# Kernel tuning notes

Measured on AMD Instinct MI355X. Metric: run time of the kernel, lower is better.

The kernel has to match this reference:

```python
import jax, jax.numpy as jnp
import numpy as np
from functools import partial

GRID = 5  # 224/32 - 2
N_ANCHORS = 3
N_BOX = GRID * GRID * N_ANCHORS  # 75


def _make_anchors():
    # faithful replication of _create_anchors (grid-index cx,cy with pixel-scale w,h)
    scales = [56, 112, 224]
    a = np.zeros((GRID, GRID, N_ANCHORS, 8), np.float32)
    for x in range(GRID):
        for y in range(GRID):
            for k in range(N_ANCHORS):
                w = h = scales[k]
                a[x, y, k] = [x - w // 2, y - h // 2, x + w // 2, y + h // 2, x, y, w, h]
    return jnp.asarray(a)

ANCHORS = _make_anchors()  # [5,5,3,8]: x0,y0,x1,y1,cx,cy,w,h


def conv2d(x, w, b, pad):
    y = jax.lax.conv_general_dilated(x, w, (1, 1), [(pad, pad), (pad, pad)],
                                     dimension_numbers=('NCHW', 'OIHW', 'NCHW'))
    return y + b[None, :, None, None]


def maxpool2(x):
    return jax.lax.reduce_window(x, -jnp.inf, jax.lax.max,
                                 (1, 1, 2, 2), (1, 1, 2, 2), 'VALID')


def deparam_bboxes(rp_reg):
    # rp_reg: [B,5,5,3,4]; anchors broadcast over batch
    aw = ANCHORS[..., 6]; ah = ANCHORS[..., 7]
    ax = ANCHORS[..., 4]; ay = ANCHORS[..., 5]
    cx = rp_reg[..., 0] * aw + ax
    cy = rp_reg[..., 1] * ah + ay
    w = jnp.exp(rp_reg[..., 2]) * aw
    h = jnp.exp(rp_reg[..., 3]) * ah
    return jnp.stack([cx - w / 2, cy - h / 2, cx + w / 2, cy + h / 2], axis=-1)


def _iou_as_written(bi, bj):
    # replicates bb_intersection_over_union EXACTLY, including the missing
    # parentheses bug: inter/areaA + areaB - inter
    xA = jnp.maximum(bi[0], bj[..., 0]); yA = jnp.maximum(bi[1], bj[..., 1])
    xB = jnp.minimum(bi[2], bj[..., 2]); yB = jnp.minimum(bi[3], bj[..., 3])
    inter = jnp.maximum(0.0, xB - xA + 1) * jnp.maximum(0.0, yB - yA + 1)
    areaA = (bi[2] - bi[0] + 1) * (bi[3] - bi[1] + 1)
    areaB = (bj[..., 2] - bj[..., 0] + 1) * (bj[..., 3] - bj[..., 1] + 1)
    return inter / areaA + areaB - inter


def nms_single(boxes, scores, thresh=0.7):
    # boxes [75,4], scores [75]; greedy suppression in score order (vectorized
    # replacement of the O(n^2) Python-loop NMS in _compute_bboxes)
    order = jnp.argsort(-scores)
    b = boxes[order]
    idx = jnp.arange(N_BOX)

    def body(i, keep):
        iou = _iou_as_written(b[i], b)          # [75]
        sup = (idx > i) & (iou > thresh) & keep[i]
        return keep & ~sup

    keep_sorted = jax.lax.fori_loop(0, N_BOX, body, jnp.ones(N_BOX, bool))
    return jnp.zeros(N_BOX, bool).at[order].set(keep_sorted)


def setup_inputs() -> dict:
    key = jax.random.key(0)
    ks = jax.random.split(key, 16)
    B = 32
    inp = {"x": jax.random.normal(ks[0], (B, 3, 224, 224), jnp.float32)}
    chans = [3, 64, 128, 256, 512, 512]
    for i in range(5):
        cin, cout = chans[i], chans[i + 1]
        std = float(np.sqrt(2.0 / (cout * 9)))  # kaiming fan_out, relu
        inp[f"fw{i}"] = jax.random.normal(ks[1 + i], (cout, cin, 3, 3), jnp.float32) * std
        inp[f"fb{i}"] = jnp.zeros((cout,), jnp.float32)
    # RPN heads: normal(0, 0.01), zero bias (per _initialize_rp_weights)
    inp["rpw_w"] = jax.random.normal(ks[6], (512, 512, 3, 3), jnp.float32) * 0.01
    inp["rpw_b"] = jnp.zeros((512,), jnp.float32)
    inp["cls_w"] = jax.random.normal(ks[7], (N_ANCHORS, 512, 1, 1), jnp.float32) * 0.01
    inp["cls_b"] = jnp.zeros((N_ANCHORS,), jnp.float32)
    inp["reg_w"] = jax.random.normal(ks[8], (4 * N_ANCHORS, 512, 1, 1), jnp.float32) * 0.01
    inp["reg_b"] = jnp.zeros((4 * N_ANCHORS,), jnp.float32)
    # classifier2: Linear(512*7*7, 20), normal(0, 0.01)
    inp["fc_w"] = jax.random.normal(ks[9], (20, 512 * 7 * 7), jnp.float32) * 0.01
    inp["fc_b"] = jnp.zeros((20,), jnp.float32)
    return inp


def reference(x, fw0, fb0, fw1, fb1, fw2, fb2, fw3, fb3, fw4, fb4,
              rpw_w, rpw_b, cls_w, cls_b, reg_w, reg_b, fc_w, fc_b):
    B = x.shape[0]
    feat = x
    for w, b in ((fw0, fb0), (fw1, fb1), (fw2, fb2), (fw3, fb3), (fw4, fb4)):
        feat = maxpool2(jax.nn.relu(conv2d(feat, w, b, pad=1)))
    # feat: [B,512,7,7]
    rp512 = jax.nn.relu(conv2d(feat, rpw_w, rpw_b, pad=0))          # [B,512,5,5]
    rp_cls = jax.nn.sigmoid(conv2d(rp512, cls_w, cls_b, pad=0))     # [B,3,5,5]
    rp_reg = conv2d(rp512, reg_w, reg_b, pad=0)                     # [B,12,5,5]
    # faithful to torch .view (row-major reshape, NOT permute)
    rp_cls = rp_cls.reshape(B, GRID, GRID, N_ANCHORS)
    rp_reg = rp_reg.reshape(B, GRID, GRID, N_ANCHORS, 4)
    bboxes = deparam_bboxes(rp_reg)                                 # [B,5,5,3,4]
    keep = jax.vmap(nms_single)(bboxes.reshape(B, N_BOX, 4),
                                rp_cls.reshape(B, N_BOX))           # [B,75] bool
    logits = feat.reshape(B, -1) @ fc_w.T + fc_b                    # [B,20]
    return logits, rp_cls, rp_reg, bboxes, keep
```

## Files before the change

### kernel.cpp

```cpp
#include <hip/hip_runtime.h>
#include <math.h>


#define OFF_LOGITS 0
#define OFF_CLS    640
#define OFF_REG    3040
#define OFF_BOXES  12640
#define OFF_KEEP   22240

constexpr int BATCH = 32;

typedef _Float16 h8 __attribute__((ext_vector_type(8)));
typedef _Float16 h4 __attribute__((ext_vector_type(4)));
typedef float    f4 __attribute__((ext_vector_type(4)));

#define MFMA16(a, b, c) __builtin_amdgcn_mfma_f32_16x16x32_f16(a, b, c, 0, 0, 0)

#if defined(__has_builtin)
#  if __has_builtin(__builtin_amdgcn_global_load_lds)
#    define HAS_GLL 1
#  endif
#endif

__device__ __forceinline__ void stage16(const _Float16* g, _Float16* lbase, int lane) {
#ifdef HAS_GLL
  __builtin_amdgcn_global_load_lds((const __attribute__((address_space(1))) void*)g,
                                   (__attribute__((address_space(3))) void*)lbase,
                                   16, 0, 0);
#else
  *reinterpret_cast<h8*>(lbase + lane * 8) = *reinterpret_cast<const h8*>(g);
#endif
}

constexpr size_t A_OFF = 0;
constexpr size_t B_OFF = 106463232;
constexpr size_t W_OFF = 161579008;
constexpr size_t P_OFF = A_OFF + 8388608;

constexpr int I0_E = 26615808;
constexpr int I1_E = 13778944;
constexpr int I2_E = 7372800;
constexpr int I3_E = 4194304;
constexpr int I4_E = 802816;

__global__ __launch_bounds__(256)
void wcvt(const float* __restrict__ src, _Float16* __restrict__ dHi,
          _Float16* __restrict__ dLo, int COUT, int CIN) {
  const int total = COUT * CIN * 9;
  for (int idx = blockIdx.x * 256 + threadIdx.x; idx < total; idx += gridDim.x * 256) {
    const int co = idx / (CIN * 9);
    const int r = idx % (CIN * 9);
    const int ci = r / 9, tap = r % 9;
    const float v = src[idx];
    const _Float16 h = (_Float16)v;
    const int o = ((tap * (CIN >> 5) + (ci >> 5)) * COUT + co) * 32 + (ci & 31);
    dHi[o] = h;
    dLo[o] = (_Float16)(v - (float)h);
  }
}

__global__ __launch_bounds__(256)
void zero_ring(_Float16* __restrict__ hi, _Float16* __restrict__ lo, int P, int C) {
  const int c8n = C / 8, cells = 4 * P - 4;
  const int tot = 32 * cells * c8n;
  for (int idx = blockIdx.x * 256 + threadIdx.x; idx < tot; idx += gridDim.x * 256) {
    const int c8 = idx % c8n;
    const int cell = (idx / c8n) % cells;
    const int n = idx / (c8n * cells);
    int y, xx;
    if (cell < 2 * P) { y = (cell < P) ? 0 : (P - 1); xx = cell % P; }
    else { const int q = cell - 2 * P; y = 1 + (q >> 1); xx = (q & 1) ? (P - 1) : 0; }
    const long o = ((long)(n * P + y) * P + xx) * C + c8 * 8;
    h8 z = {};
    *reinterpret_cast<h8*>(hi + o) = z;
    *reinterpret_cast<h8*>(lo + o) = z;
  }
}

constexpr int L0_SW   = 0;
constexpr int L0_SB   = 6912;
constexpr int L0_SIN  = 7168;
constexpr int L0_HI   = 7168;
constexpr int L0_LO   = 7168 + 36864;
constexpr int L0_LDS  = 7168 + 73728;

__global__ __launch_bounds__(256)
void conv_l0(const float* __restrict__ x, const float* __restrict__ w0,
             const float* __restrict__ b0, _Float16* __restrict__ outHi,
             _Float16* __restrict__ outLo) {
  const int bid = blockIdx.x;
  const int tx0 = (bid % 7) * 16, ty0 = ((bid / 7) % 7) * 16, n = bid / 49;
  __align__(16) __shared__ char lds[L0_LDS];
  float* sW = (float*)(lds + L0_SW);
  float* sB = (float*)(lds + L0_SB);
  float* sIn = (float*)(lds + L0_SIN);
  const int tid = threadIdx.x;
  for (int idx = tid; idx < 3 * 34 * 34; idx += 256) {
    const int ci = idx / 1156, rem = idx % 1156, r = rem / 34, cc = rem % 34;
    const int y = 2 * ty0 - 1 + r, xx = 2 * tx0 - 1 + cc;
    float v = 0.f;
    if ((unsigned)y < 224u && (unsigned)xx < 224u)
      v = x[((n * 3 + ci) * 224 + y) * 224 + xx];
    sIn[idx] = v;
  }
  for (int idx = tid; idx < 1728; idx += 256) sW[idx] = w0[idx];
  if (tid < 64) sB[tid] = b0[tid];
  __syncthreads();

  const int tpy = tid / 16, tpx = tid % 16;
  float win[3][4][4];
  #pragma unroll
  for (int ci = 0; ci < 3; ++ci)
    #pragma unroll
    for (int dr = 0; dr < 4; ++dr)
      #pragma unroll
      for (int dc = 0; dc < 4; ++dc)
        win[ci][dr][dc] = sIn[ci * 1156 + (2 * tpy + dr) * 34 + (2 * tpx + dc)];
  __syncthreads();

  for (int co4 = 0; co4 < 16; ++co4) {
    h4 hh, ll;
    #pragma unroll
    for (int j = 0; j < 4; ++j) {
      const int co = co4 * 4 + j;
      float a00 = 0.f, a01 = 0.f, a10 = 0.f, a11 = 0.f;
      #pragma unroll
      for (int ci = 0; ci < 3; ++ci)
        #pragma unroll
        for (int ky = 0; ky < 3; ++ky)
          #pragma unroll
          for (int kx = 0; kx < 3; ++kx) {
            const float wv = sW[co * 27 + ci * 9 + ky * 3 + kx];
            a00 = fmaf(win[ci][ky][kx], wv, a00);
            a01 = fmaf(win[ci][ky][kx + 1], wv, a01);
            a10 = fmaf(win[ci][ky + 1][kx], wv, a10);
            a11 = fmaf(win[ci][ky + 1][kx + 1], wv, a11);
          }
      const float p = fmaxf(fmaxf(fmaxf(a00, a01), fmaxf(a10, a11)) + sB[co], 0.f);
      const _Float16 h = (_Float16)p;
      hh[j] = h;
      ll[j] = (_Float16)(p - (float)h);
    }
    *reinterpret_cast<h4*>(lds + L0_HI + tid * 144 + co4 * 8) = hh;
    *reinterpret_cast<h4*>(lds + L0_LO + tid * 144 + co4 * 8) = ll;
  }
  __syncthreads();

  const int tr_half = tid >> 7;
  const int pixrow = (tid & 127) >> 3;
  const int ch8 = (tid & 7) * 8;
  #pragma unroll
  for (int i = 0; i < 8; ++i) {
    const int tr = 2 * i + tr_half;
    const int pix = tr * 16 + pixrow;
    const long ga = ((long)(n * 114 + ty0 + tr + 1) * 114 + tx0 + pixrow + 1) * 64 + ch8;
    *reinterpret_cast<h8*>(outHi + ga) =
        *reinterpret_cast<const h8*>(lds + L0_HI + pix * 144 + ch8 * 2);
    *reinterpret_cast<h8*>(outLo + ga) =
        *reinterpret_cast<const h8*>(lds + L0_LO + pix * 144 + ch8 * 2);
  }
}

template<int CIN, int COUT, int H, int XH, int NCOW, int STG, int SARR>
__global__ __launch_bounds__(256, 2)
void convrow(const _Float16* __restrict__ inHi, const _Float16* __restrict__ inLo,
             const _Float16* __restrict__ wHi, const _Float16* __restrict__ wLo,
             const float* __restrict__ bias, _Float16* __restrict__ outHi,
             _Float16* __restrict__ outLo) {
  constexpr int W = H, Hp = H / 2, Wp = W / 2, PW = W + 2, POW = Wp + 2;
  constexpr int KCH = CIN / 32;
  constexpr int NPH = 3 * KCH;
  constexpr int NSPW = 4 / NCOW;
  constexpr int NFULL = STG / 64;
  constexpr int TAIL = STG % 64;
  static_assert(NSPW * 64 + 3 < STG + 1, "staged rows cover shifted reads");
  __align__(16) __shared__ _Float16 sB[2][2][SARR * 32];

  const int tid = threadIdx.x;
  const int lane = tid & 63, wv = tid >> 6;
  const int c = lane & 15, kq = lane >> 4;
  const int cow = blockIdx.y * (NCOW * 64) + (wv % NCOW) * 64;
  const int spl = (wv / NCOW) * 64;
  const int xh = blockIdx.x % XH;
  const int pyn = blockIdx.x / XH;
  const int py = pyn % Hp, n = pyn / Hp;
  const int x0 = xh * 64;

  int gstage[NFULL + 1];
  #pragma unroll
  for (int i = 0; i < NFULL + 1; ++i) {
    const int sl = i * 64 + tid / 4;
    const int ry = sl & 1;
    int xx = x0 + (sl >> 1);
    if (xx > PW - 1) xx = PW - 1;
    gstage[i] = ((n * (H + 2) + 2 * py + ry) * PW + xx) * CIN +
                (((tid & 3) ^ ((sl >> 1) & 3)) * 8);
  }
  int dsoff[3][4];
  #pragma unroll
  for (int kx = 0; kx < 3; ++kx)
    #pragma unroll
    for (int nt = 0; nt < 4; ++nt) {
      const int r = spl + nt * 16 + c + 2 * kx;
      dsoff[kx][nt] = r * 32 + ((kq ^ ((r >> 1) & 3)) * 8);
    }

  #pragma unroll
  for (int i = 0; i < NFULL; ++i) {
    stage16(inHi + gstage[i], &sB[0][0][i * 2048 + wv * 512], lane);
    stage16(inLo + gstage[i], &sB[0][1][i * 2048 + wv * 512], lane);
  }
  if (TAIL && tid < TAIL * 4) {
    stage16(inHi + gstage[NFULL], &sB[0][0][NFULL * 2048], lane);
    stage16(inLo + gstage[NFULL], &sB[0][1][NFULL * 2048], lane);
  }
  __syncthreads();

  f4 acc[4][4] = {};
  int cur = 0;
  for (int ph = 0; ph < NPH; ++ph) {
    const int ky = ph / KCH, kc = ph % KCH;
    if (ph + 1 < NPH) {
      const int tb2 = ((ph + 1) / KCH) * PW * CIN + ((ph + 1) % KCH) * 32;
      #pragma unroll
      for (int i = 0; i < NFULL; ++i) {
        stage16(inHi + gstage[i] + tb2, &sB[cur ^ 1][0][i * 2048 + wv * 512], lane);
        stage16(inLo + gstage[i] + tb2, &sB[cur ^ 1][1][i * 2048 + wv * 512], lane);
      }
      if (TAIL && tid < TAIL * 4) {
        stage16(inHi + gstage[NFULL] + tb2, &sB[cur ^ 1][0][NFULL * 2048], lane);
        stage16(inLo + gstage[NFULL] + tb2, &sB[cur ^ 1][1][NFULL * 2048], lane);
      }
    }
    #pragma unroll
    for (int kx = 0; kx < 3; ++kx) {
      h8 aH[4], aL[4];
      const long abase = ((long)((ky * 3 + kx) * KCH + kc) * COUT + cow) * 32;
      #pragma unroll
      for (int mt = 0; mt < 4; ++mt) {
        const long ao = abase + (mt * 16 + c) * 32 + kq * 8;
        aH[mt] = *reinterpret_cast<const h8*>(wHi + ao);
        aL[mt] = *reinterpret_cast<const h8*>(wLo + ao);
      }
      h8 bH[4], bL[4];
      #pragma unroll
      for (int nt = 0; nt < 4; ++nt) {
        bH[nt] = *reinterpret_cast<const h8*>(&sB[cur][0][dsoff[kx][nt]]);
        bL[nt] = *reinterpret_cast<const h8*>(&sB[cur][1][dsoff[kx][nt]]);
      }
      __builtin_amdgcn_s_setprio(1);
      #pragma unroll
      for (int mt = 0; mt < 4; ++mt)
        #pragma unroll
        for (int nt = 0; nt < 4; ++nt)
          acc[mt][nt] = MFMA16(aH[mt], bH[nt], acc[mt][nt]);
      #pragma unroll
      for (int mt = 0; mt < 4; ++mt)
        #pragma unroll
        for (int nt = 0; nt < 4; ++nt)
          acc[mt][nt] = MFMA16(aH[mt], bL[nt], acc[mt][nt]);
      #pragma unroll
      for (int mt = 0; mt < 4; ++mt)
        #pragma unroll
        for (int nt = 0; nt < 4; ++nt)
          acc[mt][nt] = MFMA16(aL[mt], bH[nt], acc[mt][nt]);
      __builtin_amdgcn_s_setprio(0);
    }
    __syncthreads();
    cur ^= 1;
  }

  const int r4 = lane >> 4;
  #pragma unroll
  for (int mt = 0; mt < 4; ++mt) {
    const int co0 = cow + mt * 16 + r4 * 4;
    const f4 bi = *reinterpret_cast<const f4*>(bias + co0);
    #pragma unroll
    for (int nt = 0; nt < 4; ++nt) {
      f4 v = acc[mt][nt];
      #pragma unroll
      for (int r = 0; r < 4; ++r) {
        const float m1 = fmaxf(v[r], __shfl_xor(v[r], 1, 64));
        v[r] = fmaxf(m1, __shfl_xor(m1, 2, 64));
      }
      if ((lane & 3) == 0) {
        const int rr = spl + nt * 16 + c;
        const int pxg = xh * 32 + (rr >> 2);
        if (pxg < Wp) {
          h4 hh, ll;
          #pragma unroll
          for (int r = 0; r < 4; ++r) {
            const float p = fmaxf(v[r] + bi[r], 0.f);
            const _Float16 h = (_Float16)p;
            hh[r] = h;
            ll[r] = (_Float16)(p - (float)h);
          }
          const long oa = ((long)((n * (Hp + 2) + py + 1) * POW + pxg + 1)) * COUT + co0;
          *reinterpret_cast<h4*>(outHi + oa) = hh;
          *reinterpret_cast<h4*>(outLo + oa) = ll;
        }
      }
    }
  }
}

template<int CIN, int COUT, int H, int BCO, int BSP, int TG, int KPH, int MODE>
__global__ __launch_bounds__(256, 2)
void convpool(const _Float16* __restrict__ inHi, const _Float16* __restrict__ inLo,
              const _Float16* __restrict__ wHi, const _Float16* __restrict__ wLo,
              const float* __restrict__ bias, _Float16* __restrict__ outHi,
              _Float16* __restrict__ outLo, float* __restrict__ outF) {
  constexpr int W = H, Hp = H / 2, Wp = W / 2, PW = W + 2, POW = Wp + 2;
  constexpr int NCOW = BCO / 64, NSPW = BSP / 64;
  static_assert(NCOW * NSPW == 4, "4 waves");
  constexpr int KCH = CIN / 32;
  constexpr int NCH = TG * KCH;
  constexpr int NPH = NCH / KPH;
  static_assert(NCH % KPH == 0, "even phases");
  static_assert(KPH * 2 * (BSP / 64) == 4, "prologue vmcnt literal = 4");
  constexpr int NISS = BSP / 64;
  constexpr int SPTOT = 32 * H * W;
  constexpr int TSZ = BSP * 32;
  __align__(16) __shared__ _Float16 sB[3 * 2 * KPH * TSZ];
  #define TIDX(buf, hl, j) ((((buf) * 2 + (hl)) * KPH + (j)) * TSZ)

  const int tid = threadIdx.x;
  const int lane = tid & 63, wv = tid >> 6;
  const int c = lane & 15, kq = lane >> 4;
  const int cow = blockIdx.y * BCO + (wv % NCOW) * 64;
  const int spl = (wv / NCOW) * 64;
  const int sblk = blockIdx.x * BSP;
  const int tap0 = (TG == 9) ? 0 : blockIdx.z * TG;

  int gstage[NISS];
  #pragma unroll
  for (int i = 0; i < NISS; ++i) {
    const int sl = i * 64 + tid / 4;
    const int sg = sblk + sl;
    const int ry = sg & 1, tt = sg >> 1;
    const int x = tt % W, u = tt / W;
    const int py = u % Hp, n = u / Hp;
    gstage[i] = ((n * (H + 2) + 2 * py + ry) * PW + x) * CIN +
                (((tid & 3) ^ ((sl >> 1) & 3)) * 8);
  }
  int dsoff[4];
  #pragma unroll
  for (int nt = 0; nt < 4; ++nt) {
    const int row = spl + nt * 16 + c;
    dsoff[nt] = row * 32 + ((kq ^ ((row >> 1) & 3)) * 8);
  }

  #pragma unroll
  for (int pp = 0; pp < 2; ++pp) {
    #pragma unroll
    for (int j = 0; j < KPH; ++j) {
      const int ch = pp * KPH + j;
      const int tap = tap0 + ch / KCH, kc = ch % KCH;
      const int tb = ((tap / 3) * PW + (tap % 3)) * CIN + kc * 32;
      #pragma unroll
      for (int i = 0; i < NISS; ++i) {
        stage16(inHi + gstage[i] + tb, &sB[TIDX(pp, 0, j) + i * 2048 + wv * 512], lane);
        stage16(inLo + gstage[i] + tb, &sB[TIDX(pp, 1, j) + i * 2048 + wv * 512], lane);
      }
    }
  }
  __builtin_amdgcn_sched_barrier(0);
  asm volatile("s_waitcnt vmcnt(4)" ::: "memory");
  __builtin_amdgcn_sched_barrier(0);
  __builtin_amdgcn_s_barrier();
  __builtin_amdgcn_sched_barrier(0);

  f4 acc[4][4] = {};
  for (int ph = 0; ph < NPH; ++ph) {
    const int bp = ph % 3;
    h8 aH[KPH][4], aL[KPH][4];
    #pragma unroll
    for (int j = 0; j < KPH; ++j) {
      const int ch = ph * KPH + j;
      const int tap = tap0 + ch / KCH;
      const int kc = ch % KCH;
      const long abase = ((long)(tap * KCH + kc) * COUT + cow) * 32;
      #pragma unroll
      for (int mt = 0; mt < 4; ++mt) {
        const long ao = abase + (mt * 16 + c) * 32 + kq * 8;
        aH[j][mt] = *reinterpret_cast<const h8*>(wHi + ao);
        aL[j][mt] = *reinterpret_cast<const h8*>(wLo + ao);
      }
    }
    __builtin_amdgcn_sched_barrier(0);
    if (ph + 2 < NPH) {
      const int bs = (ph + 2) % 3;
      #pragma unroll
      for (int j2 = 0; j2 < KPH; ++j2) {
        const int ch2 = (ph + 2) * KPH + j2;
        const int tap2 = tap0 + ch2 / KCH;
        const int tb2 = ((tap2 / 3) * PW + (tap2 % 3)) * CIN + (ch2 % KCH) * 32;
        #pragma unroll
        for (int i = 0; i < NISS; ++i) {
          stage16(inHi + gstage[i] + tb2,
                  &sB[TIDX(bs, 0, j2) + i * 2048 + wv * 512], lane);
          stage16(inLo + gstage[i] + tb2,
                  &sB[TIDX(bs, 1, j2) + i * 2048 + wv * 512], lane);
        }
      }
    }
    __builtin_amdgcn_sched_barrier(0);
    #pragma unroll
    for (int j = 0; j < KPH; ++j) {
      h8 bH[4], bL[4];
      #pragma unroll
      for (int nt = 0; nt < 4; ++nt) {
        bH[nt] = *reinterpret_cast<const h8*>(&sB[TIDX(bp, 0, j) + dsoff[nt]]);
        bL[nt] = *reinterpret_cast<const h8*>(&sB[TIDX(bp, 1, j) + dsoff[nt]]);
      }
      __builtin_amdgcn_s_setprio(1);
      #pragma unroll
      for (int mt = 0; mt < 4; ++mt)
        #pragma unroll
        for (int nt = 0; nt < 4; ++nt)
          acc[mt][nt] = MFMA16(aH[j][mt], bH[nt], acc[mt][nt]);
      #pragma unroll
      for (int mt = 0; mt < 4; ++mt)
        #pragma unroll
        for (int nt = 0; nt < 4; ++nt)
          acc[mt][nt] = MFMA16(aH[j][mt], bL[nt], acc[mt][nt]);
      #pragma unroll
      for (int mt = 0; mt < 4; ++mt)
        #pragma unroll
        for (int nt = 0; nt < 4; ++nt)
          acc[mt][nt] = MFMA16(aL[j][mt], bH[nt], acc[mt][nt]);
      __builtin_amdgcn_s_setprio(0);
    }
    __builtin_amdgcn_sched_barrier(0);
    __builtin_amdgcn_s_barrier();
    __builtin_amdgcn_sched_barrier(0);
  }
  #undef TIDX

  const int r4 = lane >> 4;
  if (MODE == 1) {
    #pragma unroll
    for (int mt = 0; mt < 4; ++mt) {
      const int co0 = cow + mt * 16 + r4 * 4;
      #pragma unroll
      for (int nt = 0; nt < 4; ++nt) {
        const int s = sblk + spl + nt * 16 + c;
        *reinterpret_cast<f4*>(outF + ((long)blockIdx.z * SPTOT + s) * COUT + co0) =
            acc[mt][nt];
      }
    }
  } else {
    #pragma unroll
    for (int mt = 0; mt < 4; ++mt) {
      const int co0 = cow + mt * 16 + r4 * 4;
      const f4 bi = *reinterpret_cast<const f4*>(bias + co0);
      #pragma unroll
      for (int nt = 0; nt < 4; ++nt) {
        f4 v = acc[mt][nt];
        #pragma unroll
        for (int r = 0; r < 4; ++r) {
          const float m1 = fmaxf(v[r], __shfl_xor(v[r], 1, 64));
          v[r] = fmaxf(m1, __shfl_xor(m1, 2, 64));
        }
        if ((lane & 3) == 0) {
          const int s = sblk + spl + nt * 16 + c;
          const int ps = s >> 2;
          const int n = ps / (Hp * Wp), rem = ps % (Hp * Wp);
          const int py = rem / Wp, px = rem % Wp;
          h4 hh, ll;
          #pragma unroll
          for (int r = 0; r < 4; ++r) {
            const float p = fmaxf(v[r] + bi[r], 0.f);
            const _Float16 h = (_Float16)p;
            hh[r] = h;
            ll[r] = (_Float16)(p - (float)h);
          }
          const long oa = ((long)((n * (Hp + 2) + py + 1) * POW + px + 1)) * COUT + co0;
          *reinterpret_cast<h4*>(outHi + oa) = hh;
          *reinterpret_cast<h4*>(outLo + oa) = ll;
        }
      }
    }
  }
}

__global__ __launch_bounds__(256)
void l4_finish(const float* __restrict__ part, const float* __restrict__ bias,
               _Float16* __restrict__ I4h, _Float16* __restrict__ I4l,
               float* __restrict__ feat) {
  const int t = blockIdx.x * 256 + threadIdx.x;
  if (t >= 1568 * 128) return;
  const int co0 = (t % 128) * 4, p = t / 128;
  f4 m;
  #pragma unroll
  for (int q = 0; q < 4; ++q) {
    const long s = 4L * p + q;
    f4 v = *reinterpret_cast<const f4*>(part + s * 512 + co0);
    v += *reinterpret_cast<const f4*>(part + (6272 + s) * 512 + co0);
    v += *reinterpret_cast<const f4*>(part + (12544 + s) * 512 + co0);
    if (q == 0) m = v;
    else {
      #pragma unroll
      for (int r = 0; r < 4; ++r) m[r] = fmaxf(m[r], v[r]);
    }
  }
  const f4 bi = *reinterpret_cast<const f4*>(bias + co0);
  h4 hh, ll;
  const int n = p / 49, pix = p % 49;
  #pragma unroll
  for (int r = 0; r < 4; ++r) {
    const float pv = fmaxf(m[r] + bi[r], 0.f);
    const _Float16 h = (_Float16)pv;
    hh[r] = h;
    ll[r] = (_Float16)(pv - (float)h);
    feat[((long)(n * 512 + co0 + r)) * 49 + pix] = pv;
  }
  *reinterpret_cast<h4*>(I4h + (long)p * 512 + co0) = hh;
  *reinterpret_cast<h4*>(I4l + (long)p * 512 + co0) = ll;
}

__global__ __launch_bounds__(256)
void rpn_partial(const _Float16* __restrict__ inHi, const _Float16* __restrict__ inLo,
                 const _Float16* __restrict__ wHi, const _Float16* __restrict__ wLo,
                 float* __restrict__ part) {
  const int lane = threadIdx.x & 63, wv = threadIdx.x >> 6;
  const int cow = blockIdx.y * 128 + wv * 32;
  const int sblk = blockIdx.x * 64;
  const int tap = blockIdx.z, ky = tap / 3, kx = tap % 3;
  const int c = lane & 15, kq = lane >> 4;

  int baseB[4];
  #pragma unroll
  for (int nt = 0; nt < 4; ++nt) {
    int s = sblk + nt * 16 + c;
    if (s > 799) s = 799;
    const int n = s / 25, pix = s % 25, py = pix / 5, px = pix % 5;
    baseB[nt] = ((n * 7 + py + ky) * 7 + px + kx) * 512;
  }

  f4 acc[2][4] = {};
  for (int kch = 0; kch < 16; ++kch) {
    h8 aH[2], aL[2], bH[4], bL[4];
    const long abase = ((long)(tap * 16 + kch) * 512 + cow) * 32;
    #pragma unroll
    for (int mt = 0; mt < 2; ++mt) {
      const long ao = abase + (mt * 16 + c) * 32 + kq * 8;
      aH[mt] = *reinterpret_cast<const h8*>(wHi + ao);
      aL[mt] = *reinterpret_cast<const h8*>(wLo + ao);
    }
    #pragma unroll
    for (int nt = 0; nt < 4; ++nt) {
      const int bo = baseB[nt] + kch * 32 + kq * 8;
      bH[nt] = *reinterpret_cast<const h8*>(inHi + bo);
      bL[nt] = *reinterpret_cast<const h8*>(inLo + bo);
    }
    #pragma unroll
    for (int mt = 0; mt < 2; ++mt)
      #pragma unroll
      for (int nt = 0; nt < 4; ++nt)
        acc[mt][nt] = MFMA16(aH[mt], bH[nt], acc[mt][nt]);
    #pragma unroll
    for (int mt = 0; mt < 2; ++mt)
      #pragma unroll
      for (int nt = 0; nt < 4; ++nt)
        acc[mt][nt] = MFMA16(aH[mt], bL[nt], acc[mt][nt]);
    #pragma unroll
    for (int mt = 0; mt < 2; ++mt)
      #pragma unroll
      for (int nt = 0; nt < 4; ++nt)
        acc[mt][nt] = MFMA16(aL[mt], bH[nt], acc[mt][nt]);
  }

  const int r4 = lane >> 4;
  #pragma unroll
  for (int mt = 0; mt < 2; ++mt) {
    const int co0 = cow + mt * 16 + r4 * 4;
    #pragma unroll
    for (int nt = 0; nt < 4; ++nt) {
      const int s = sblk + nt * 16 + c;
      if (s < 800)
        *reinterpret_cast<f4*>(part + ((long)tap * 800 + s) * 512 + co0) = acc[mt][nt];
    }
  }
}

__global__ __launch_bounds__(256)
void rpn_finish(const float* __restrict__ part, const float* __restrict__ bias,
                float* __restrict__ rp512) {
  const int t = blockIdx.x * 256 + threadIdx.x;
  if (t >= 800 * 128) return;
  const int co0 = (t % 128) * 4, s = t / 128;
  f4 acc = *reinterpret_cast<const f4*>(bias + co0);
  #pragma unroll
  for (int g = 0; g < 9; ++g)
    acc += *reinterpret_cast<const f4*>(part + ((long)g * 800 + s) * 512 + co0);
  f4 o;
  #pragma unroll
  for (int r = 0; r < 4; ++r) o[r] = fmaxf(acc[r], 0.f);
  *reinterpret_cast<f4*>(rp512 + (long)s * 512 + co0) = o;
}

__global__ __launch_bounds__(256)
void heads_kernel(const float* __restrict__ rp512,
                  const float* __restrict__ cls_w, const float* __restrict__ cls_b,
                  const float* __restrict__ reg_w, const float* __restrict__ reg_b,
                  float* __restrict__ out) {
  const int idx = blockIdx.x * 256 + threadIdx.x;
  if (idx >= 32 * 25 * 15) return;
  const int o = idx % 15, pix = (idx / 15) % 25, n = idx / 375;
  const float* __restrict__ ip = rp512 + ((long)(n * 25 + pix)) * 512;
  const float* __restrict__ wvp = (o < 3) ? (cls_w + o * 512) : (reg_w + (o - 3) * 512);
  float acc = 0.f;
  for (int k = 0; k < 512; k += 4) {
    const f4 a = *reinterpret_cast<const f4*>(ip + k);
    const f4 b = *reinterpret_cast<const f4*>(wvp + k);
    acc = fmaf(a[0], b[0], acc); acc = fmaf(a[1], b[1], acc);
    acc = fmaf(a[2], b[2], acc); acc = fmaf(a[3], b[3], acc);
  }
  if (o < 3) {
    acc += cls_b[o];
    out[OFF_CLS + n * 75 + o * 25 + pix] = 1.f / (1.f + expf(-acc));
  } else {
    acc += reg_b[o - 3];
    out[OFF_REG + n * 300 + (o - 3) * 25 + pix] = acc;
  }
}

__global__ __launch_bounds__(256)
void fc_kernel(const float* __restrict__ feat, const float* __restrict__ fw,
               const float* __restrict__ fb, float* __restrict__ out) {
  const int n = blockIdx.x, j = blockIdx.y;
  const float* __restrict__ ip = feat + (long)n * 25088;
  const float* __restrict__ wj = fw + (long)j * 25088;
  float acc = 0.f;
  for (int k = threadIdx.x * 4; k < 25088; k += 1024) {
    const f4 a = *reinterpret_cast<const f4*>(ip + k);
    const f4 b = *reinterpret_cast<const f4*>(wj + k);
    acc = fmaf(a[0], b[0], acc); acc = fmaf(a[1], b[1], acc);
    acc = fmaf(a[2], b[2], acc); acc = fmaf(a[3], b[3], acc);
  }
  #pragma unroll
  for (int m = 32; m >= 1; m >>= 1) acc += __shfl_xor(acc, m, 64);
  __shared__ float red[4];
  const int wv = threadIdx.x >> 6;
  if ((threadIdx.x & 63) == 0) red[wv] = acc;
  __syncthreads();
  if (threadIdx.x == 0)
    out[OFF_LOGITS + n * 20 + j] = red[0] + red[1] + red[2] + red[3] + fb[j];
}

__global__ __launch_bounds__(128)
void bbox_nms_kernel(float* __restrict__ out) {
  const int n = blockIdx.x;
  const int t = threadIdx.x;
  __shared__ float bx0[75], by0[75], bx1[75], by1[75], area[75], sc[75];
  __shared__ int rank_s[75], order_s[75], keep_s[75];

  if (t < 75) {
    const int g1 = t / 15, g2 = (t / 3) % 5, a = t % 3;
    const float aw = (a == 0) ? 56.f : (a == 1 ? 112.f : 224.f);
    const float r0 = out[OFF_REG + n * 300 + 4 * t + 0];
    const float r1 = out[OFF_REG + n * 300 + 4 * t + 1];
    const float r2 = out[OFF_REG + n * 300 + 4 * t + 2];
    const float r3 = out[OFF_REG + n * 300 + 4 * t + 3];
    const float cx = r0 * aw + (float)g1;
    const float cy = r1 * aw + (float)g2;
    const float w_ = expf(r2) * aw;
    const float h_ = expf(r3) * aw;
    const float x0 = cx - 0.5f * w_, y0 = cy - 0.5f * h_;
    const float x1 = cx + 0.5f * w_, y1 = cy + 0.5f * h_;
    bx0[t] = x0; by0[t] = y0; bx1[t] = x1; by1[t] = y1;
    area[t] = (x1 - x0 + 1.f) * (y1 - y0 + 1.f);
    out[OFF_BOXES + n * 300 + 4 * t + 0] = x0;
    out[OFF_BOXES + n * 300 + 4 * t + 1] = y0;
    out[OFF_BOXES + n * 300 + 4 * t + 2] = x1;
    out[OFF_BOXES + n * 300 + 4 * t + 3] = y1;
    sc[t] = out[OFF_CLS + n * 75 + t];
    keep_s[t] = 1;
  }
  __syncthreads();
  if (t < 75) {
    const float si = sc[t];
    int rk = 0;
    for (int j = 0; j < 75; ++j) {
      const float sj = sc[j];
      rk += (sj > si) || (sj == si && j < t);
    }
    rank_s[t] = rk;
    order_s[rk] = t;
  }
  __syncthreads();
  for (int i = 0; i < 74; ++i) {
    if (keep_s[i]) {
      const int bi = order_s[i];
      if (t > i && t < 75) {
        const int bj = order_s[t];
        const float xA = fmaxf(bx0[bi], bx0[bj]);
        const float yA = fmaxf(by0[bi], by0[bj]);
        const float xB = fminf(bx1[bi], bx1[bj]);
        const float yB = fminf(by1[bi], by1[bj]);
        const float inter = fmaxf(0.f, xB - xA + 1.f) * fmaxf(0.f, yB - yA + 1.f);
        const float iou = inter / area[bi] + area[bj] - inter;
        if (iou > 0.7f) keep_s[t] = 0;
      }
    }
    __syncthreads();
  }
  if (t < 75) out[OFF_KEEP + n * 75 + t] = keep_s[rank_s[t]] ? 1.f : 0.f;
}

extern "C" void kernel_launch(void* const* d_in, const int* in_sizes, int n_in,
                              void* d_out, int out_size, void* d_ws, size_t ws_size,
                              hipStream_t stream) {
  (void)in_sizes; (void)n_in; (void)out_size; (void)ws_size;
  const float* x     = (const float*)d_in[0];
  const float* fw0   = (const float*)d_in[1];
  const float* fb0   = (const float*)d_in[2];
  const float* fw1   = (const float*)d_in[3];
  const float* fb1   = (const float*)d_in[4];
  const float* fw2   = (const float*)d_in[5];
  const float* fb2   = (const float*)d_in[6];
  const float* fw3   = (const float*)d_in[7];
  const float* fb3   = (const float*)d_in[8];
  const float* fw4   = (const float*)d_in[9];
  const float* fb4   = (const float*)d_in[10];
  const float* rpw_w = (const float*)d_in[11];
  const float* rpw_b = (const float*)d_in[12];
  const float* cls_w = (const float*)d_in[13];
  const float* cls_b = (const float*)d_in[14];
  const float* reg_w = (const float*)d_in[15];
  const float* reg_b = (const float*)d_in[16];
  const float* fc_w  = (const float*)d_in[17];
  const float* fc_b  = (const float*)d_in[18];
  float* out = (float*)d_out;
  char* ws = (char*)d_ws;

  _Float16* I0h = (_Float16*)(ws + A_OFF);
  _Float16* I0l = I0h + I0_E;
  _Float16* I1h = (_Float16*)(ws + B_OFF);
  _Float16* I1l = I1h + I1_E;
  _Float16* I2h = (_Float16*)(ws + A_OFF);
  _Float16* I2l = I2h + I2_E;
  _Float16* I3h = (_Float16*)(ws + B_OFF);
  _Float16* I3l = I3h + I3_E;
  _Float16* I4h = (_Float16*)(ws + A_OFF);
  _Float16* I4l = I4h + I4_E;
  float* feat  = (float*)(ws + A_OFF + (size_t)I4_E * 4);
  float* rp512 = (float*)(ws + A_OFF + (size_t)I4_E * 4 + 3211264);
  float* part  = (float*)(ws + P_OFF);

  _Float16* w1h = (_Float16*)(ws + W_OFF);                _Float16* w1l = w1h + 73728;
  _Float16* w2h = (_Float16*)(ws + W_OFF + 294912);       _Float16* w2l = w2h + 294912;
  _Float16* w3h = (_Float16*)(ws + W_OFF + 1474560);      _Float16* w3l = w3h + 1179648;
  _Float16* w4h = (_Float16*)(ws + W_OFF + 6193152);      _Float16* w4l = w4h + 2359296;
  _Float16* wrh = (_Float16*)(ws + W_OFF + 15630336);     _Float16* wrl = wrh + 2359296;

  wcvt<<<(73728 + 255) / 256, 256, 0, stream>>>(fw1, w1h, w1l, 128, 64);
  wcvt<<<(294912 + 255) / 256, 256, 0, stream>>>(fw2, w2h, w2l, 256, 128);
  wcvt<<<(1179648 + 255) / 256, 256, 0, stream>>>(fw3, w3h, w3l, 512, 256);
  wcvt<<<(2359296 + 255) / 256, 256, 0, stream>>>(fw4, w4h, w4l, 512, 512);
  wcvt<<<(2359296 + 255) / 256, 256, 0, stream>>>(rpw_w, wrh, wrl, 512, 512);

  zero_ring<<<512, 256, 0, stream>>>(I0h, I0l, 114, 64);
  zero_ring<<<512, 256, 0, stream>>>(I1h, I1l, 58, 128);

  conv_l0<<<32 * 49, 256, 0, stream>>>(x, fw0, fb0, I0h, I0l);

  convrow<64, 128, 112, 2, 2, 132, 136><<<dim3(32 * 56 * 2, 1), 256, 0, stream>>>(
      I0h, I0l, w1h, w1l, fb1, I1h, I1l);
  zero_ring<<<512, 256, 0, stream>>>(I2h, I2l, 30, 256);
  convrow<128, 256, 56, 1, 2, 132, 136><<<dim3(32 * 28, 2), 256, 0, stream>>>(
      I1h, I1l, w2h, w2l, fb2, I2h, I2l);
  zero_ring<<<512, 256, 0, stream>>>(I3h, I3l, 16, 512);
  convrow<256, 512, 28, 1, 4, 68, 72><<<dim3(32 * 14, 2), 256, 0, stream>>>(
      I2h, I2l, w3h, w3l, fb3, I3h, I3l);
  convpool<512, 512, 14, 256, 64, 3, 2, 1><<<dim3(98, 2, 3), 256, 0, stream>>>(
      I3h, I3l, w4h, w4l, nullptr, nullptr, nullptr, part);
  l4_finish<<<(1568 * 128 + 255) / 256, 256, 0, stream>>>(part, fb4, I4h, I4l, feat);

  rpn_partial<<<dim3(13, 4, 9), 256, 0, stream>>>(I4h, I4l, wrh, wrl, part);
  rpn_finish<<<(800 * 128 + 255) / 256, 256, 0, stream>>>(part, rpw_b, rp512);

  heads_kernel<<<(12000 + 255) / 256, 256, 0, stream>>>(rp512, cls_w, cls_b, reg_w, reg_b, out);
  fc_kernel<<<dim3(32, 20), 256, 0, stream>>>(feat, fc_w, fc_b, out);
  bbox_nms_kernel<<<BATCH, 128, 0, stream>>>(out);
}
```

Baseline: 865.9 us.

## Widen convrow tiles so each block covers full COUT and row width

The convrow kernel drops the x-half and output-channel grid splits, so each block now computes a full pooled output row across all output channels. Each wave holds 8 M-tiles (128 channels), which raises reuse of each LDS-staged input fragment and cuts repeated staging of the same input rows across blocks. The MFMA passes are split into a bH phase and a bL phase with sched barriers to limit live registers. The cost is a larger accumulator footprint, more register pressure and far fewer blocks, which may underfill the GPU on the deeper layers. Layer 1 also needs a bigger LDS staging area.

```diff
diff --git a/kernel.cpp b/kernel.cpp
--- a/kernel.cpp
+++ b/kernel.cpp
@@ -161,7 +161,7 @@
   }
 }
 
-template<int CIN, int COUT, int H, int XH, int NCOW, int STG, int SARR>
+template<int CIN, int COUT, int H, int NCOW, int STG, int SARR>
 __global__ __launch_bounds__(256, 2)
 void convrow(const _Float16* __restrict__ inHi, const _Float16* __restrict__ inLo,
              const _Float16* __restrict__ wHi, const _Float16* __restrict__ wLo,
@@ -169,29 +169,27 @@
              _Float16* __restrict__ outLo) {
   constexpr int W = H, Hp = H / 2, Wp = W / 2, PW = W + 2, POW = Wp + 2;
   constexpr int KCH = CIN / 32;
-  constexpr int NPH = 3 * KCH;
+  constexpr int NCH = 3 * KCH;
   constexpr int NSPW = 4 / NCOW;
   constexpr int NFULL = STG / 64;
   constexpr int TAIL = STG % 64;
-  static_assert(NSPW * 64 + 3 < STG + 1, "staged rows cover shifted reads");
+  static_assert(NCOW * 128 == COUT, "full COUT per block");
+  static_assert(NSPW * 64 + 3 < STG, "staged rows cover shifted reads");
   __align__(16) __shared__ _Float16 sB[2][2][SARR * 32];
 
   const int tid = threadIdx.x;
   const int lane = tid & 63, wv = tid >> 6;
   const int c = lane & 15, kq = lane >> 4;
-  const int cow = blockIdx.y * (NCOW * 64) + (wv % NCOW) * 64;
+  const int cow = (wv % NCOW) * 128;
   const int spl = (wv / NCOW) * 64;
-  const int xh = blockIdx.x % XH;
-  const int pyn = blockIdx.x / XH;
-  const int py = pyn % Hp, n = pyn / Hp;
-  const int x0 = xh * 64;
+  const int py = blockIdx.x % Hp, n = blockIdx.x / Hp;
 
   int gstage[NFULL + 1];
   #pragma unroll
   for (int i = 0; i < NFULL + 1; ++i) {
     const int sl = i * 64 + tid / 4;
     const int ry = sl & 1;
-    int xx = x0 + (sl >> 1);
+    int xx = sl >> 1;
     if (xx > PW - 1) xx = PW - 1;
     gstage[i] = ((n * (H + 2) + 2 * py + ry) * PW + xx) * CIN +
                 (((tid & 3) ^ ((sl >> 1) & 3)) * 8);
@@ -216,12 +214,23 @@
   }
   __syncthreads();
 
-  f4 acc[4][4] = {};
+  f4 acc[8][4] = {};
   int cur = 0;
-  for (int ph = 0; ph < NPH; ++ph) {
-    const int ky = ph / KCH, kc = ph % KCH;
-    if (ph + 1 < NPH) {
-      const int tb2 = ((ph + 1) / KCH) * PW * CIN + ((ph + 1) % KCH) * 32;
+  for (int ch = 0; ch < NCH; ++ch) {
+    const int ky = ch / KCH, kc = ch % KCH;
+    h8 aH[8], aL[8];
+    {
+      const long abase = ((long)((ky * 3 + 0) * KCH + kc) * COUT + cow) * 32;
+      #pragma unroll
+      for (int mt = 0; mt < 8; ++mt) {
+        const long ao = abase + (mt * 16 + c) * 32 + kq * 8;
+        aH[mt] = *reinterpret_cast<const h8*>(wHi + ao);
+        aL[mt] = *reinterpret_cast<const h8*>(wLo + ao);
+      }
+    }
+    __builtin_amdgcn_sched_barrier(0);
+    if (ch + 1 < NCH) {
+      const int tb2 = ((ch + 1) / KCH) * PW * CIN + ((ch + 1) % KCH) * 32;
       #pragma unroll
       for (int i = 0; i < NFULL; ++i) {
         stage16(inHi + gstage[i] + tb2, &sB[cur ^ 1][0][i * 2048 + wv * 512], lane);
@@ -232,39 +241,52 @@
         stage16(inLo + gstage[NFULL] + tb2, &sB[cur ^ 1][1][NFULL * 2048], lane);
       }
     }
+    __builtin_amdgcn_sched_barrier(0);
     #pragma unroll
     for (int kx = 0; kx < 3; ++kx) {
-      h8 aH[4], aL[4];
-      const long abase = ((long)((ky * 3 + kx) * KCH + kc) * COUT + cow) * 32;
-      #pragma unroll
-      for (int mt = 0; mt < 4; ++mt) {
-        const long ao = abase + (mt * 16 + c) * 32 + kq * 8;
-        aH[mt] = *reinterpret_cast<const h8*>(wHi + ao);
-        aL[mt] = *reinterpret_cast<const h8*>(wLo + ao);
-      }
-      h8 bH[4], bL[4];
-      #pragma unroll
-      for (int nt = 0; nt < 4; ++nt) {
-        bH[nt] = *reinterpret_cast<const h8*>(&sB[cur][0][dsoff[kx][nt]]);
-        bL[nt] = *reinterpret_cast<const h8*>(&sB[cur][1][dsoff[kx][nt]]);
-      }
-      __builtin_amdgcn_s_setprio(1);
-      #pragma unroll
-      for (int mt = 0; mt < 4; ++mt)
+      if (kx > 0) {
+        const long abase = ((long)((ky * 3 + kx) * KCH + kc) * COUT + cow) * 32;
+        #pragma unroll
+        for (int mt = 0; mt < 8; ++mt) {
+          const long ao = abase + (mt * 16 + c) * 32 + kq * 8;
+          aH[mt] = *reinterpret_cast<const h8*>(wHi + ao);
+          aL[mt] = *reinterpret_cast<const h8*>(wLo + ao);
+        }
+        __builtin_amdgcn_sched_barrier(0);
+      }
+      {
+        h8 bH[4];
         #pragma unroll
         for (int nt = 0; nt < 4; ++nt)
-          acc[mt][nt] = MFMA16(aH[mt], bH[nt], acc[mt][nt]);
-      #pragma unroll
-      for (int mt = 0; mt < 4; ++mt)
+          bH[nt] = *reinterpret_cast<const h8*>(&sB[cur][0][dsoff[kx][nt]]);
+        __builtin_amdgcn_s_setprio(1);
+        #pragma unroll
+        for (int mt = 0; mt < 8; ++mt)
+          #pragma unroll
+          for (int nt = 0; nt < 4; ++nt)
+            acc[mt][nt] = MFMA16(aH[mt], bH[nt], acc[mt][nt]);
+        #pragma unroll
+        for (int mt = 0; mt < 8; ++mt)
+          #pragma unroll
+          for (int nt = 0; nt < 4; ++nt)
+            acc[mt][nt] = MFMA16(aL[mt], bH[nt], acc[mt][nt]);
+        __builtin_amdgcn_s_setprio(0);
+      }
+      __builtin_amdgcn_sched_barrier(0);
+      {
+        h8 bL[4];
         #pragma unroll
         for (int nt = 0; nt < 4; ++nt)
-          acc[mt][nt] = MFMA16(aH[mt], bL[nt], acc[mt][nt]);
-      #pragma unroll
-      for (int mt = 0; mt < 4; ++mt)
-        #pragma unroll
-        for (int nt = 0; nt < 4; ++nt)
-          acc[mt][nt] = MFMA16(aL[mt], bH[nt], acc[mt][nt]);
-      __builtin_amdgcn_s_setprio(0);
+          bL[nt] = *reinterpret_cast<const h8*>(&sB[cur][1][dsoff[kx][nt]]);
+        __builtin_amdgcn_s_setprio(1);
+        #pragma unroll
+        for (int mt = 0; mt < 8; ++mt)
+          #pragma unroll
+          for (int nt = 0; nt < 4; ++nt)
+            acc[mt][nt] = MFMA16(aH[mt], bL[nt], acc[mt][nt]);
+        __builtin_amdgcn_s_setprio(0);
+      }
+      __builtin_amdgcn_sched_barrier(0);
     }
     __syncthreads();
     cur ^= 1;
@@ -272,7 +294,7 @@
 
   const int r4 = lane >> 4;
   #pragma unroll
-  for (int mt = 0; mt < 4; ++mt) {
+  for (int mt = 0; mt < 8; ++mt) {
     const int co0 = cow + mt * 16 + r4 * 4;
     const f4 bi = *reinterpret_cast<const f4*>(bias + co0);
     #pragma unroll
@@ -285,7 +307,7 @@
       }
       if ((lane & 3) == 0) {
         const int rr = spl + nt * 16 + c;
-        const int pxg = xh * 32 + (rr >> 2);
+        const int pxg = rr >> 2;
         if (pxg < Wp) {
           h4 hh, ll;
           #pragma unroll
@@ -766,13 +788,13 @@
 
   conv_l0<<<32 * 49, 256, 0, stream>>>(x, fw0, fb0, I0h, I0l);
 
-  convrow<64, 128, 112, 2, 2, 132, 136><<<dim3(32 * 56 * 2, 1), 256, 0, stream>>>(
+  convrow<64, 128, 112, 1, 260, 264><<<dim3(32 * 56), 256, 0, stream>>>(
       I0h, I0l, w1h, w1l, fb1, I1h, I1l);
   zero_ring<<<512, 256, 0, stream>>>(I2h, I2l, 30, 256);
-  convrow<128, 256, 56, 1, 2, 132, 136><<<dim3(32 * 28, 2), 256, 0, stream>>>(
+  convrow<128, 256, 56, 2, 132, 136><<<dim3(32 * 28), 256, 0, stream>>>(
       I1h, I1l, w2h, w2l, fb2, I2h, I2l);
   zero_ring<<<512, 256, 0, stream>>>(I3h, I3l, 16, 512);
-  convrow<256, 512, 28, 1, 4, 68, 72><<<dim3(32 * 14, 2), 256, 0, stream>>>(
+  convrow<256, 512, 28, 4, 68, 72><<<dim3(32 * 14), 256, 0, stream>>>(
       I2h, I2l, w3h, w3l, fb3, I3h, I3l);
   convpool<512, 512, 14, 256, 64, 3, 2, 1><<<dim3(98, 2, 3), 256, 0, stream>>>(
       I3h, I3l, w4h, w4l, nullptr, nullptr, nullptr, part);
```

Result: slower. 894.1 us (+3.3%).
